# Kernel optimization log

Measured on AMD Instinct MI355X. Metric: run time of the kernel, lower is better.

## Reference

```python
import jax, jax.numpy as jnp
import numpy as np

B, I, O, K, H = 64, 16384, 1024, 5, 16  # batch, input_dim, output_dim, num_basis, basis hidden


def setup_inputs() -> dict:
    key = jax.random.key(0)
    ks = jax.random.split(key, 6)
    x = jax.random.normal(ks[0], (B, I), dtype=jnp.float32)
    # Per-basis 1->16->1 MLP params (Linear(1,16): weight [16,1] stored squeezed as [K,16])
    w1 = jax.random.normal(ks[1], (K, H), dtype=jnp.float32) * (1.0)
    b1 = jax.random.normal(ks[2], (K, H), dtype=jnp.float32) * 0.1
    w2 = jax.random.normal(ks[3], (K, H), dtype=jnp.float32) * (1.0 / np.sqrt(H))
    b2 = jax.random.normal(ks[4], (K,), dtype=jnp.float32) * 0.1
    # KAN mixing weights [output_dim, input_dim, num_basis]
    W = jax.random.normal(ks[5], (O, I, K), dtype=jnp.float32)
    return {"x": x, "w1": w1, "b1": b1, "w2": w2, "b2": b2, "W": W}


def reference(x, w1, b1, w2, b2, W):
    # basis MLP index per input feature (cyclic reuse of the num_basis MLPs,
    # matching intended basis_functions[in_dim % num_basis])
    K_ = w1.shape[0]
    idx = jnp.arange(x.shape[1]) % K_            # [I], static
    W1, B1 = w1[idx], b1[idx]                    # [I,H]
    W2, B2 = w2[idx], b2[idx]                    # [I,H], [I]
    # basis_i(x[:, i]) = w2_i @ silu(w1_i * x + b1_i) + b2_i
    h = jax.nn.silu(x[:, :, None] * W1[None] + B1[None])   # [B,I,H]
    basis = jnp.einsum("bih,ih->bi", h, W2) + B2[None]     # [B,I]
    # out[b,o] = sum_i sum_k W[o,i,k] * basis[b,i]  (basis broadcasts over k)
    Wsum = W.sum(axis=-1)                                  # [O,I]
    return jnp.einsum("bi,oi->bo", basis, Wsum)            # [B,O]
```

## Files before the change

### kernel.cpp

```cpp
#include <hip/hip_runtime.h>
#include <hip/hip_bf16.h>

#define B_DIM 64
#define I_DIM 16384
#define O_DIM 1024
#define K_BASIS 5
#define H_DIM 16
#define IK (I_DIM * K_BASIS)

typedef __attribute__((ext_vector_type(8))) short short8;
typedef __attribute__((ext_vector_type(4))) float f32x4;

__global__ __launch_bounds__(256)
void basis_kernel(const float* __restrict__ x,
                  const float* __restrict__ w1,
                  const float* __restrict__ b1,
                  const float* __restrict__ w2,
                  const float* __restrict__ b2,
                  __hip_bfloat16* __restrict__ basis) {
    __shared__ float4 pk[K_BASIS][H_DIM + 1];
    __shared__ float pb2[K_BASIS];
    const int t = threadIdx.x;
    if (t < K_BASIS * H_DIM) {
        const int k = t / H_DIM, h = t % H_DIM;
        pk[k][h] = float4{w1[t], b1[t], w2[t], 0.f};
        if (t < K_BASIS) pb2[t] = b2[t];
    }
    __syncthreads();

    const int gid = blockIdx.x * 256 + t;
    const int i8 = gid % (I_DIM / 8);
    const int b  = gid / (I_DIM / 8);
    const int i0 = i8 * 8;

    const float4* xp = reinterpret_cast<const float4*>(x + (size_t)b * I_DIM + i0);
    float4 xa = xp[0];
    float4 xb = xp[1];
    float xs[8] = {xa.x, xa.y, xa.z, xa.w, xb.x, xb.y, xb.z, xb.w};

    __hip_bfloat16 res[8];
#pragma unroll
    for (int j = 0; j < 8; ++j) {
        const int idx = (i0 + j) % K_BASIS;
        const float xv = xs[j];
        float acc = 0.f;
#pragma unroll
        for (int h = 0; h < H_DIM; ++h) {
            const float4 p = pk[idx][h];
            float a = fmaf(xv, p.x, p.y);
            float s = a * __builtin_amdgcn_rcpf(1.f + __expf(-a));
            acc = fmaf(s, p.z, acc);
        }
        res[j] = __float2bfloat16(acc + pb2[idx]);
    }
    *reinterpret_cast<short8*>(basis + (size_t)b * I_DIM + i0) =
        *reinterpret_cast<short8*>(res);
}

#define NT 16
#define CI 128
#define KSPLIT 8
#define NCHUNK (I_DIM / KSPLIT / CI)
#define LDBS 136

#define PUBLISH() do {                                                  \
        asm volatile("s_waitcnt lgkmcnt(0)" ::: "memory");              \
        __builtin_amdgcn_s_barrier();                                   \
        asm volatile("" ::: "memory");                                  \
    } while (0)

__global__ __launch_bounds__(256)
void kan_gemm(const float* __restrict__ W,
              const __hip_bfloat16* __restrict__ basis,
              float* __restrict__ out) {
    __shared__ float4 smem[1024];
    __hip_bfloat16* Bs0 = reinterpret_cast<__hip_bfloat16*>(smem);
    __hip_bfloat16* Bs1 = Bs0 + NT * LDBS;
    float* red = reinterpret_cast<float*>(smem);

    const int t    = threadIdx.x;
    const int lane = t & 63;
    const int wv   = t >> 6;
    const int col  = lane & 15;
    const int kgrp = lane >> 4;
    const int o0   = blockIdx.x * NT;
    const int i00  = blockIdx.y * (CI * NCHUNK);

    const int srow = t >> 4;
    const int sseg = t & 15;
    const float* wbase = W + (size_t)(o0 + srow) * IK + (size_t)i00 * K_BASIS
                           + sseg * 40;
    const __hip_bfloat16* abase = basis + i00 + wv * 32 + kgrp * 8;

    float4 ra[10], rb[10];
    short8 af[4];

#define ISSUE(R, c) do {                                                \
        const float4* p = reinterpret_cast<const float4*>(              \
            wbase + (size_t)(c) * (CI * K_BASIS));                      \
        _Pragma("unroll") for (int q = 0; q < 10; ++q) R[q] = p[q];     \
    } while (0)

#define COMMIT(BS, R) do {                                              \
        float ws[8] = {0.f,0.f,0.f,0.f,0.f,0.f,0.f,0.f};                \
        _Pragma("unroll") for (int q = 0; q < 10; ++q) {                \
            ws[(4*q+0)/5] += R[q].x;                                    \
            ws[(4*q+1)/5] += R[q].y;                                    \
            ws[(4*q+2)/5] += R[q].z;                                    \
            ws[(4*q+3)/5] += R[q].w;                                    \
        }                                                               \
        __hip_bfloat16 wb8[8];                                          \
        _Pragma("unroll") for (int u = 0; u < 8; ++u)                   \
            wb8[u] = __float2bfloat16(ws[u]);                           \
        *reinterpret_cast<short8*>(&BS[srow * LDBS + sseg * 8]) =       \
            *reinterpret_cast<short8*>(wb8);                            \
    } while (0)

#define AFLOAD(c) do {                                                  \
        _Pragma("unroll") for (int m = 0; m < 4; ++m)                   \
            af[m] = *reinterpret_cast<const short8*>(                   \
                abase + (size_t)(m * 16 + col) * I_DIM + (c) * CI);     \
    } while (0)

#define COMPUTE(BS) do {                                                \
        const short8 bfr = *reinterpret_cast<const short8*>(            \
            &BS[col * LDBS + wv * 32 + kgrp * 8]);                      \
        _Pragma("unroll") for (int m = 0; m < 4; ++m)                   \
            acc[m] = __builtin_amdgcn_mfma_f32_16x16x32_bf16(           \
                af[m], bfr, acc[m], 0, 0, 0);                           \
    } while (0)

    f32x4 acc[4] = {f32x4{0,0,0,0}, f32x4{0,0,0,0}, f32x4{0,0,0,0}, f32x4{0,0,0,0}};

    ISSUE(ra, 0);
    ISSUE(rb, 1);
    COMMIT(Bs0, ra);
    PUBLISH();

#pragma unroll
    for (int cc = 0; cc < NCHUNK; cc += 2) {
        AFLOAD(cc);
        __builtin_amdgcn_sched_barrier(0);
        if (cc + 2 < NCHUNK) ISSUE(ra, cc + 2);
        COMMIT(Bs1, rb);
        COMPUTE(Bs0);
        PUBLISH();
        AFLOAD(cc + 1);
        __builtin_amdgcn_sched_barrier(0);
        if (cc + 3 < NCHUNK) ISSUE(rb, cc + 3);
        if (cc + 2 < NCHUNK) COMMIT(Bs0, ra);
        COMPUTE(Bs1);
        if (cc + 2 < NCHUNK) PUBLISH();
    }
    PUBLISH();

#pragma unroll
    for (int m = 0; m < 4; ++m)
#pragma unroll
        for (int j = 0; j < 4; ++j)
            red[wv * 1024 + (m * 16 + kgrp * 4 + j) * 16 + col] = acc[m][j];
    PUBLISH();

    const float4 v0 = *reinterpret_cast<const float4*>(&red[0 * 1024 + t * 4]);
    const float4 v1 = *reinterpret_cast<const float4*>(&red[1 * 1024 + t * 4]);
    const float4 v2 = *reinterpret_cast<const float4*>(&red[2 * 1024 + t * 4]);
    const float4 v3 = *reinterpret_cast<const float4*>(&red[3 * 1024 + t * 4]);
    const float s[4] = {v0.x + v1.x + v2.x + v3.x, v0.y + v1.y + v2.y + v3.y,
                        v0.z + v1.z + v2.z + v3.z, v0.w + v1.w + v2.w + v3.w};
    const int brow = t >> 2;
    const int c4   = (t & 3) * 4;
#pragma unroll
    for (int k = 0; k < 4; ++k)
        atomicAdd(&out[(size_t)brow * O_DIM + o0 + c4 + k], s[k]);

#undef ISSUE
#undef COMMIT
#undef AFLOAD
#undef COMPUTE
}

extern "C" void kernel_launch(void* const* d_in, const int* in_sizes, int n_in,
                              void* d_out, int out_size, void* d_ws, size_t ws_size,
                              hipStream_t stream) {
    const float* x  = (const float*)d_in[0];
    const float* w1 = (const float*)d_in[1];
    const float* b1 = (const float*)d_in[2];
    const float* w2 = (const float*)d_in[3];
    const float* b2 = (const float*)d_in[4];
    const float* W  = (const float*)d_in[5];
    float* out = (float*)d_out;
    __hip_bfloat16* basis = (__hip_bfloat16*)d_ws;

    hipMemsetAsync(d_out, 0, (size_t)out_size * sizeof(float), stream);

    basis_kernel<<<dim3((B_DIM * I_DIM / 8) / 256), dim3(256), 0, stream>>>(
        x, w1, b1, w2, b2, basis);

    dim3 grid(O_DIM / NT, KSPLIT);
    kan_gemm<<<grid, dim3(256), 0, stream>>>(W, basis, out);
}
```

Measured before the change: 92.01 us.

## Stage raw fp32 W tiles in swizzled LDS and reduce basis sum on read

The W-tile load is remapped so each thread issues flat, coalesced 16-byte loads across the 16-row tile instead of 40 contiguous floats per thread. The raw fp32 data goes into LDS with an XOR swizzle, and the k-sum plus bf16 conversion moves into the compute step, where each thread reads its fragment straight from LDS. The goal is better global coalescing and fewer bank conflicts. In exchange, LDS grows to about 80KB for the double buffer and more LDS traffic lands on the critical path. Launch bounds now also ask for 2 blocks per CU.

```diff
diff --git a/kernel.cpp b/kernel.cpp
--- a/kernel.cpp
+++ b/kernel.cpp
@@ -61,7 +61,8 @@
 #define CI 128
 #define KSPLIT 8
 #define NCHUNK (I_DIM / KSPLIT / CI)
-#define LDBS 136
+#define ROWB (CI * K_BASIS * 4)
+#define BUFB (NT * ROWB)
 
 #define PUBLISH() do {                                                  \
         asm volatile("s_waitcnt lgkmcnt(0)" ::: "memory");              \
@@ -69,14 +70,14 @@
         asm volatile("" ::: "memory");                                  \
     } while (0)
 
-__global__ __launch_bounds__(256)
+__global__ __launch_bounds__(256, 2)
 void kan_gemm(const float* __restrict__ W,
               const __hip_bfloat16* __restrict__ basis,
               float* __restrict__ out) {
-    __shared__ float4 smem[1024];
-    __hip_bfloat16* Bs0 = reinterpret_cast<__hip_bfloat16*>(smem);
-    __hip_bfloat16* Bs1 = Bs0 + NT * LDBS;
-    float* red = reinterpret_cast<float*>(smem);
+    __shared__ float4 smem[2 * BUFB / 16];
+    char* const Bs0 = reinterpret_cast<char*>(smem);
+    char* const Bs1 = Bs0 + BUFB;
+    float* const red = reinterpret_cast<float*>(smem);
 
     const int t    = threadIdx.x;
     const int lane = t & 63;
@@ -86,34 +87,36 @@
     const int o0   = blockIdx.x * NT;
     const int i00  = blockIdx.y * (CI * NCHUNK);
 
-    const int srow = t >> 4;
-    const int sseg = t & 15;
-    const float* wbase = W + (size_t)(o0 + srow) * IK + (size_t)i00 * K_BASIS
-                           + sseg * 40;
-    const __hip_bfloat16* abase = basis + i00 + wv * 32 + kgrp * 8;
+    int goff[10], loff[10];
+#pragma unroll
+    for (int q = 0; q < 10; ++q) {
+        const int flat = t + 256 * q;
+        const int row  = flat / 160;
+        const int u    = flat - row * 160;
+        goff[q] = row * (IK * 4) + u * 16;
+        loff[q] = (row * 160 + (u ^ (row & 7))) * 16;
+    }
+    int rdoff[10];
+#pragma unroll
+    for (int q = 0; q < 10; ++q)
+        rdoff[q] = (col * 160 + ((wv * 40 + kgrp * 10 + q) ^ (col & 7))) * 16;
+
+    const char* const wbase = reinterpret_cast<const char*>(W)
+                            + (size_t)o0 * (IK * 4) + (size_t)i00 * 20;
+    const __hip_bfloat16* const abase = basis + i00 + wv * 32 + kgrp * 8;
 
     float4 ra[10], rb[10];
     short8 af[4];
 
 #define ISSUE(R, c) do {                                                \
-        const float4* p = reinterpret_cast<const float4*>(              \
-            wbase + (size_t)(c) * (CI * K_BASIS));                      \
-        _Pragma("unroll") for (int q = 0; q < 10; ++q) R[q] = p[q];     \
+        _Pragma("unroll") for (int q = 0; q < 10; ++q)                  \
+            R[q] = *reinterpret_cast<const float4*>(                    \
+                wbase + (size_t)(c) * ROWB + goff[q]);                  \
     } while (0)
 
 #define COMMIT(BS, R) do {                                              \
-        float ws[8] = {0.f,0.f,0.f,0.f,0.f,0.f,0.f,0.f};                \
-        _Pragma("unroll") for (int q = 0; q < 10; ++q) {                \
-            ws[(4*q+0)/5] += R[q].x;                                    \
-            ws[(4*q+1)/5] += R[q].y;                                    \
-            ws[(4*q+2)/5] += R[q].z;                                    \
-            ws[(4*q+3)/5] += R[q].w;                                    \
-        }                                                               \
-        __hip_bfloat16 wb8[8];                                          \
-        _Pragma("unroll") for (int u = 0; u < 8; ++u)                   \
-            wb8[u] = __float2bfloat16(ws[u]);                           \
-        *reinterpret_cast<short8*>(&BS[srow * LDBS + sseg * 8]) =       \
-            *reinterpret_cast<short8*>(wb8);                            \
+        _Pragma("unroll") for (int q = 0; q < 10; ++q)                  \
+            *reinterpret_cast<float4*>((BS) + loff[q]) = R[q];          \
     } while (0)
 
 #define AFLOAD(c) do {                                                  \
@@ -123,8 +126,19 @@
     } while (0)
 
 #define COMPUTE(BS) do {                                                \
-        const short8 bfr = *reinterpret_cast<const short8*>(            \
-            &BS[col * LDBS + wv * 32 + kgrp * 8]);                      \
+        float ws[8] = {0.f,0.f,0.f,0.f,0.f,0.f,0.f,0.f};                \
+        _Pragma("unroll") for (int q = 0; q < 10; ++q) {                \
+            const float4 v = *reinterpret_cast<const float4*>(          \
+                (BS) + rdoff[q]);                                       \
+            ws[(4*q+0)/5] += v.x;                                       \
+            ws[(4*q+1)/5] += v.y;                                       \
+            ws[(4*q+2)/5] += v.z;                                       \
+            ws[(4*q+3)/5] += v.w;                                       \
+        }                                                               \
+        __hip_bfloat16 wb8[8];                                          \
+        _Pragma("unroll") for (int u2 = 0; u2 < 8; ++u2)                \
+            wb8[u2] = __float2bfloat16(ws[u2]);                         \
+        const short8 bfr = *reinterpret_cast<short8*>(wb8);             \
         _Pragma("unroll") for (int m = 0; m < 4; ++m)                   \
             acc[m] = __builtin_amdgcn_mfma_f32_16x16x32_bf16(           \
                 af[m], bfr, acc[m], 0, 0, 0);                           \
```

Result: slower. 169.2 us (+83.9%).

## Raise GEMM split-K with per-wave direct W loads and a deterministic reduce kernel

Applied to the files above, without the earlier changes.

Split-K rises from 8 to 32 slices, and each wave now loads its own W columns straight into registers and feeds them to MFMA, with no LDS staging or barriers inside the main loop. Per-block partial tiles are written to workspace and summed by a new reduce kernel, which replaces the memset plus atomicAdd accumulation. The goal is more blocks and memory parallelism for streaming the 335MB W, along with shorter per-block pipelines and no LDS synchronisation. The costs are an extra kernel launch, a round trip of partials through global memory, and lane access patterns to W that may coalesce less well than before.

```diff
diff --git a/kernel.cpp b/kernel.cpp
--- a/kernel.cpp
+++ b/kernel.cpp
@@ -58,25 +58,15 @@
 }
 
 #define NT 16
-#define CI 128
-#define KSPLIT 8
-#define NCHUNK (I_DIM / KSPLIT / CI)
-#define LDBS 136
+#define CI 32
+#define KSPLIT 32
+#define NC 4
 
-#define PUBLISH() do {                                                  \
-        asm volatile("s_waitcnt lgkmcnt(0)" ::: "memory");              \
-        __builtin_amdgcn_s_barrier();                                   \
-        asm volatile("" ::: "memory");                                  \
-    } while (0)
-
-__global__ __launch_bounds__(256)
+__global__ __launch_bounds__(256, 3)
 void kan_gemm(const float* __restrict__ W,
               const __hip_bfloat16* __restrict__ basis,
-              float* __restrict__ out) {
-    __shared__ float4 smem[1024];
-    __hip_bfloat16* Bs0 = reinterpret_cast<__hip_bfloat16*>(smem);
-    __hip_bfloat16* Bs1 = Bs0 + NT * LDBS;
-    float* red = reinterpret_cast<float*>(smem);
+              float* __restrict__ P) {
+    __shared__ float red[4 * 1024];
 
     const int t    = threadIdx.x;
     const int lane = t & 63;
@@ -84,24 +74,29 @@
     const int col  = lane & 15;
     const int kgrp = lane >> 4;
     const int o0   = blockIdx.x * NT;
-    const int i00  = blockIdx.y * (CI * NCHUNK);
+    const int ibase = blockIdx.y * (4 * NC * CI) + wv * (NC * CI);
 
-    const int srow = t >> 4;
-    const int sseg = t & 15;
-    const float* wbase = W + (size_t)(o0 + srow) * IK + (size_t)i00 * K_BASIS
-                           + sseg * 40;
-    const __hip_bfloat16* abase = basis + i00 + wv * 32 + kgrp * 8;
+    const float* const wlane = W + (size_t)(o0 + col) * IK
+                                 + (size_t)(ibase + kgrp * 8) * K_BASIS;
+    const __hip_bfloat16* const abase = basis + ibase + kgrp * 8;
 
     float4 ra[10], rb[10];
-    short8 af[4];
+    short8 afa[4], afb[4];
+    f32x4 acc[4] = {f32x4{0,0,0,0}, f32x4{0,0,0,0}, f32x4{0,0,0,0}, f32x4{0,0,0,0}};
 
 #define ISSUE(R, c) do {                                                \
         const float4* p = reinterpret_cast<const float4*>(              \
-            wbase + (size_t)(c) * (CI * K_BASIS));                      \
+            wlane + (c) * (CI * K_BASIS));                              \
         _Pragma("unroll") for (int q = 0; q < 10; ++q) R[q] = p[q];     \
     } while (0)
 
-#define COMMIT(BS, R) do {                                              \
+#define AFLOAD(AF, c) do {                                              \
+        _Pragma("unroll") for (int m = 0; m < 4; ++m)                   \
+            AF[m] = *reinterpret_cast<const short8*>(                   \
+                abase + (size_t)(m * 16 + col) * I_DIM + (c) * CI);     \
+    } while (0)
+
+#define STEP(R, AF) do {                                                \
         float ws[8] = {0.f,0.f,0.f,0.f,0.f,0.f,0.f,0.f};                \
         _Pragma("unroll") for (int q = 0; q < 10; ++q) {                \
             ws[(4*q+0)/5] += R[q].x;                                    \
@@ -112,71 +107,58 @@
         __hip_bfloat16 wb8[8];                                          \
         _Pragma("unroll") for (int u = 0; u < 8; ++u)                   \
             wb8[u] = __float2bfloat16(ws[u]);                           \
-        *reinterpret_cast<short8*>(&BS[srow * LDBS + sseg * 8]) =       \
-            *reinterpret_cast<short8*>(wb8);                            \
+        const short8 bfr = *reinterpret_cast<short8*>(wb8);             \
+        _Pragma("unroll") for (int m = 0; m < 4; ++m)                   \
+            acc[m] = __builtin_amdgcn_mfma_f32_16x16x32_bf16(           \
+                AF[m], bfr, acc[m], 0, 0, 0);                           \
     } while (0)
 
-#define AFLOAD(c) do {                                                  \
-        _Pragma("unroll") for (int m = 0; m < 4; ++m)                   \
-            af[m] = *reinterpret_cast<const short8*>(                   \
-                abase + (size_t)(m * 16 + col) * I_DIM + (c) * CI);     \
-    } while (0)
-
-#define COMPUTE(BS) do {                                                \
-        const short8 bfr = *reinterpret_cast<const short8*>(            \
-            &BS[col * LDBS + wv * 32 + kgrp * 8]);                      \
-        _Pragma("unroll") for (int m = 0; m < 4; ++m)                   \
-            acc[m] = __builtin_amdgcn_mfma_f32_16x16x32_bf16(           \
-                af[m], bfr, acc[m], 0, 0, 0);                           \
-    } while (0)
-
-    f32x4 acc[4] = {f32x4{0,0,0,0}, f32x4{0,0,0,0}, f32x4{0,0,0,0}, f32x4{0,0,0,0}};
-
-    ISSUE(ra, 0);
-    ISSUE(rb, 1);
-    COMMIT(Bs0, ra);
-    PUBLISH();
-
-#pragma unroll
-    for (int cc = 0; cc < NCHUNK; cc += 2) {
-        AFLOAD(cc);
-        __builtin_amdgcn_sched_barrier(0);
-        if (cc + 2 < NCHUNK) ISSUE(ra, cc + 2);
-        COMMIT(Bs1, rb);
-        COMPUTE(Bs0);
-        PUBLISH();
-        AFLOAD(cc + 1);
-        __builtin_amdgcn_sched_barrier(0);
-        if (cc + 3 < NCHUNK) ISSUE(rb, cc + 3);
-        if (cc + 2 < NCHUNK) COMMIT(Bs0, ra);
-        COMPUTE(Bs1);
-        if (cc + 2 < NCHUNK) PUBLISH();
-    }
-    PUBLISH();
+    ISSUE(ra, 0); AFLOAD(afa, 0);
+    ISSUE(rb, 1); AFLOAD(afb, 1);
+    STEP(ra, afa);
+    ISSUE(ra, 2); AFLOAD(afa, 2);
+    STEP(rb, afb);
+    ISSUE(rb, 3); AFLOAD(afb, 3);
+    STEP(ra, afa);
+    STEP(rb, afb);
 
 #pragma unroll
     for (int m = 0; m < 4; ++m)
 #pragma unroll
         for (int j = 0; j < 4; ++j)
             red[wv * 1024 + (m * 16 + kgrp * 4 + j) * 16 + col] = acc[m][j];
-    PUBLISH();
+    __syncthreads();
 
     const float4 v0 = *reinterpret_cast<const float4*>(&red[0 * 1024 + t * 4]);
     const float4 v1 = *reinterpret_cast<const float4*>(&red[1 * 1024 + t * 4]);
     const float4 v2 = *reinterpret_cast<const float4*>(&red[2 * 1024 + t * 4]);
     const float4 v3 = *reinterpret_cast<const float4*>(&red[3 * 1024 + t * 4]);
-    const float s[4] = {v0.x + v1.x + v2.x + v3.x, v0.y + v1.y + v2.y + v3.y,
-                        v0.z + v1.z + v2.z + v3.z, v0.w + v1.w + v2.w + v3.w};
-    const int brow = t >> 2;
-    const int c4   = (t & 3) * 4;
-#pragma unroll
-    for (int k = 0; k < 4; ++k)
-        atomicAdd(&out[(size_t)brow * O_DIM + o0 + c4 + k], s[k]);
+    const float4 s = {v0.x + v1.x + v2.x + v3.x, v0.y + v1.y + v2.y + v3.y,
+                      v0.z + v1.z + v2.z + v3.z, v0.w + v1.w + v2.w + v3.w};
+    *reinterpret_cast<float4*>(
+        P + ((size_t)(blockIdx.y * 64 + blockIdx.x) << 10) + t * 4) = s;
 
 #undef ISSUE
-#undef COMMIT
 #undef AFLOAD
-#undef COMPUTE
+#undef STEP
+}
+
+__global__ __launch_bounds__(256)
+void reduce_kernel(const float* __restrict__ P, float* __restrict__ out) {
+    const int idx = (blockIdx.x * 256 + threadIdx.x) * 4;
+    const int b  = idx >> 10;
+    const int o  = idx & 1023;
+    const int ox = o >> 4;
+    const int c0 = o & 15;
+
+    f32x4 s = {0.f, 0.f, 0.f, 0.f};
+#pragma unroll
+    for (int g = 0; g < KSPLIT; ++g) {
+        const float4 v = *reinterpret_cast<const float4*>(
+            P + ((size_t)(g * 64 + ox) << 10) + b * 16 + c0);
+        s[0] += v.x; s[1] += v.y; s[2] += v.z; s[3] += v.w;
+    }
+    *reinterpret_cast<f32x4*>(out + idx) = s;
 }
 
 extern "C" void kernel_launch(void* const* d_in, const int* in_sizes, int n_in,
@@ -189,13 +171,14 @@
     const float* b2 = (const float*)d_in[4];
     const float* W  = (const float*)d_in[5];
     float* out = (float*)d_out;
+
     __hip_bfloat16* basis = (__hip_bfloat16*)d_ws;
-
-    hipMemsetAsync(d_out, 0, (size_t)out_size * sizeof(float), stream);
+    float* P = (float*)((char*)d_ws + (2 << 20));
 
     basis_kernel<<<dim3((B_DIM * I_DIM / 8) / 256), dim3(256), 0, stream>>>(
         x, w1, b1, w2, b2, basis);
 
-    dim3 grid(O_DIM / NT, KSPLIT);
-    kan_gemm<<<grid, dim3(256), 0, stream>>>(W, basis, out);
+    kan_gemm<<<dim3(O_DIM / NT, KSPLIT), dim3(256), 0, stream>>>(W, basis, P);
+
+    reduce_kernel<<<dim3(B_DIM * O_DIM / 4 / 256), dim3(256), 0, stream>>>(P, out);
 }
```

New measurement: 143.7 us. 56.2% more time.
